# Performance work log

Measured on AMD Instinct MI355X. Metric: run time of the kernel, lower is better.

Reference implementation:

```python
import jax, jax.numpy as jnp
import numpy as np

C = 1.0            # curvature
SEG = 24           # segment_length
S = 14             # lookback // SEG = window_size
PRED_SEGS = 4      # pred_len // SEG
DECAY = 0.9
EPS = 1e-7

# ---- Poincare ball ops ----
def _norm(x):
    return jnp.sqrt(jnp.maximum(jnp.sum(x * x, -1, keepdims=True), EPS * EPS))

def project(x, c=C):
    max_n = (1.0 - 1e-5) / jnp.sqrt(c)
    n = _norm(x)
    return jnp.where(n > max_n, x * (max_n / n), x)

def mobius_add(x, y, c=C):
    x2 = jnp.sum(x * x, -1, keepdims=True)
    y2 = jnp.sum(y * y, -1, keepdims=True)
    xy = jnp.sum(x * y, -1, keepdims=True)
    num = (1 + 2 * c * xy + c * y2) * x + (1 - c * x2) * y
    den = 1 + 2 * c * xy + c * c * x2 * y2
    return num / jnp.maximum(den, 1e-15)

def logmap(x, y, c=C):
    sc = jnp.sqrt(c)
    w = mobius_add(-x, y, c)
    wn = _norm(w)
    lam = 2.0 / jnp.maximum(1.0 - c * jnp.sum(x * x, -1, keepdims=True), EPS)
    return (2.0 / (sc * lam)) * jnp.arctanh(jnp.clip(sc * wn, 0.0, 1.0 - 1e-6)) * w / wn

def expmap(x, v, c=C):
    sc = jnp.sqrt(c)
    vn = _norm(v)
    lam = 2.0 / jnp.maximum(1.0 - c * jnp.sum(x * x, -1, keepdims=True), EPS)
    second = jnp.tanh(sc * lam * vn / 2.0) * v / (sc * vn)
    return project(mobius_add(x, second, c), c)

def expmap0(v, c=C):
    sc = jnp.sqrt(c)
    vn = _norm(v)
    return project(jnp.tanh(sc * vn) * v / (sc * vn), c)

def logmap0(y, c=C):
    sc = jnp.sqrt(c)
    yn = _norm(y)
    return jnp.arctanh(jnp.clip(sc * yn, 0.0, 1.0 - 1e-6)) * y / (sc * yn)


def setup_inputs() -> dict:
    key = jax.random.key(0)
    ks = jax.random.split(key, 16)
    B, L, F = 64, 336, 64
    D, H = 256, 512
    s = 0.02
    inp = {
        "trend": jax.random.normal(ks[0], (B, L, F), jnp.float32),
        "coarse": jax.random.normal(ks[1], (B, L, F), jnp.float32),
        "fine": jax.random.normal(ks[2], (B, L, F), jnp.float32),
        "resid": jax.random.normal(ks[3], (B, L, F), jnp.float32),
        # segment embedding (shared across channels & components)
        "W_emb": jax.random.normal(ks[4], (SEG, D), jnp.float32) * s,
        "b_emb": jnp.zeros((D,), jnp.float32),
        # hyperbolic dynamics MLP: [logmap0(z_last), velocity] -> tangent update
        "W1": jax.random.normal(ks[5], (2 * D, H), jnp.float32) * s,
        "b1": jnp.zeros((H,), jnp.float32),
        "W2": jax.random.normal(ks[6], (H, D), jnp.float32) * s,
        "b2": jnp.zeros((D,), jnp.float32),
        # reconstruction head: tangent -> segment of SEG values
        "Wr1": jax.random.normal(ks[7], (D, H), jnp.float32) * s,
        "br1": jnp.zeros((H,), jnp.float32),
        "Wr2": jax.random.normal(ks[8], (H, SEG), jnp.float32) * s,
        "br2": jnp.zeros((SEG,), jnp.float32),
    }
    return inp


def reference(trend, coarse, fine, resid, W_emb, b_emb, W1, b1, W2, b2, Wr1, br1, Wr2, br2):
    B, L, F = trend.shape
    BF = B * F

    def fold(x):  # [B,L,F] -> [B*F, S, SEG]  (channel-independent)
        return x.transpose(0, 2, 1).reshape(BF, S, SEG)

    def embed(xseg):  # segment -> point on Poincare ball
        return expmap0(jnp.tanh(xseg @ W_emb + b_emb))

    combined = fold(trend + coarse + fine + resid)
    # z_all: [BF, 5, S, D] -- combined, trend, coarse, fine, resid
    z_all = jnp.stack(
        [embed(combined), embed(fold(trend)), embed(fold(coarse)),
         embed(fold(fine)), embed(fold(resid))], axis=1)

    # decayed velocity weights: most recent interval gets decay^0
    w = jnp.power(DECAY, jnp.arange(S - 2, -1, -1).astype(jnp.float32))
    w = w / jnp.sum(w)

    preds = []
    for _ in range(PRED_SEGS):
        # per-interval logmap velocities over the window, all 5 components at once
        vlog = logmap(z_all[:, :, :-1, :], z_all[:, :, 1:, :])   # [BF,5,S-1,D]
        vel = jnp.sum(vlog * w[None, None, :, None], axis=2)      # [BF,5,D]
        z_last = z_all[:, :, -1, :]                               # [BF,5,D]
        # dynamics: tangent-space MLP, step via expmap at z_last
        h = jnp.tanh(jnp.concatenate([logmap0(z_last), vel], -1) @ W1 + b1)
        z_next = expmap(z_last, h @ W2 + b2)                      # [BF,5,D]
        # reconstruct segment from tangent at origin
        r = jax.nn.relu(logmap0(z_next) @ Wr1 + br1) @ Wr2 + br2  # [BF,5,SEG]
        preds.append(r)
        z_all = jnp.concatenate([z_all[:, :, 1:, :], z_next[:, :, None, :]], axis=2)

    out = jnp.stack(preds, axis=2)                  # [BF,5,PRED_SEGS,SEG]
    out = out.reshape(B, F, 5, PRED_SEGS * SEG)     # [B,F,5,pred_len]
    return jnp.transpose(out, (2, 0, 3, 1))         # [5,B,pred_len,F]
```

## Files before the change

kernel.cpp:

```cpp
#include <hip/hip_runtime.h>
#include <cstddef>

#define NSEQ 20480
#define EPSf 1e-7f
#define MAXN 0.99999f
#define MAXN2 (0.99999f * 0.99999f)
#define QCLIP (1.f - MAXN2)
#define GS_CLIP 6.1030949f

typedef __attribute__((ext_vector_type(8))) short bf16x8;
typedef __attribute__((ext_vector_type(4))) float f32x4;

__device__ __forceinline__ unsigned short f2bf(float x) {
  unsigned u = __float_as_uint(x);
  u += 0x7FFF + ((u >> 16) & 1);
  return (unsigned short)(u >> 16);
}
__device__ __forceinline__ float bf2f(unsigned short h) {
  return __uint_as_float(((unsigned)h) << 16);
}
__device__ __forceinline__ void gload16(const void* g, void* l) {
  __builtin_amdgcn_global_load_lds(
      (const __attribute__((address_space(1))) void*)g,
      (__attribute__((address_space(3))) void*)l, 16, 0, 0);
}
__device__ __forceinline__ float fast_exp(float a) {
  return exp2f(a * 1.44269504f);
}
__device__ __forceinline__ float fast_tanh(float a) {
  float e = fast_exp(2.f * a);
  return 1.f - 2.f * __builtin_amdgcn_rcpf(e + 1.f);
}
__device__ __forceinline__ float fast_atanh(float x) {
  return 0.34657359f * log2f((1.f + x) * __builtin_amdgcn_rcpf(1.f - x));
}
__device__ __forceinline__ float sech2f(float a) {
  float u = fast_exp(-2.f * a);
  float om = 1.f + u;
  return 4.f * u * __builtin_amdgcn_rcpf(om * om);
}


__global__ __launch_bounds__(256) void fold_transpose(
    const float* __restrict__ t, const float* __restrict__ c,
    const float* __restrict__ f, const float* __restrict__ r,
    float* __restrict__ XT)
{
  __shared__ float tile[4][56][65];
  const int b = blockIdx.x, l0 = blockIdx.y * 56;
  const int tid = threadIdx.x;
  const int fi = tid & 63, lr0 = tid >> 6;
#pragma unroll
  for (int i = 0; i < 14; ++i) {
    int lr = lr0 + i * 4;
    size_t idx = ((size_t)b * 336 + l0 + lr) * 64 + fi;
    tile[0][lr][fi] = t[idx];
    tile[1][lr][fi] = c[idx];
    tile[2][lr][fi] = f[idx];
    tile[3][lr][fi] = r[idx];
  }
  __syncthreads();
#pragma unroll
  for (int ch = 0; ch < 5; ++ch) {
    for (int i = 0; i < 14; ++i) {
      int idx2 = i * 256 + tid;
      int ff = idx2 / 56, ll = idx2 % 56;
      float v;
      if (ch == 0) v = tile[0][ll][ff] + tile[1][ll][ff] + tile[2][ll][ff] + tile[3][ll][ff];
      else v = tile[ch - 1][ll][ff];
      XT[((size_t)ch * 4096 + (b << 6) + ff) * 336 + l0 + ll] = v;
    }
  }
}

__global__ __launch_bounds__(256) void conv_weight(
    const float* __restrict__ W, unsigned short* __restrict__ Wh, unsigned short* __restrict__ Wl,
    int K, int N, int Nsrc)
{
  int idx = blockIdx.x * 256 + threadIdx.x;
  if (idx >= K * N) return;
  int k = idx / N, n = idx % N;
  float x = (n < Nsrc) ? W[(size_t)k * Nsrc + n] : 0.f;
  unsigned short h = f2bf(x);
  size_t o = ((size_t)(k >> 3) * N + n) * 8 + (k & 7);
  Wh[o] = h;
  if (Wl) Wl[o] = f2bf(x - bf2f(h));
}

__global__ __launch_bounds__(256) void conv_wemb(
    const float* __restrict__ W_emb, unsigned short* __restrict__ WgH, unsigned short* __restrict__ WgL)
{
  int idx = blockIdx.x * 256 + threadIdx.x;
  if (idx >= 16 * 64 * 8) return;
  int j = idx & 7, ln = (idx >> 3) & 63, T = idx >> 9;
  int k = 8 * (ln >> 4) + j, n = T * 16 + (ln & 15);
  float x = (k < 24) ? W_emb[(size_t)k * 256 + n] : 0.f;
  unsigned short h = f2bf(x);
  WgH[idx] = h;
  WgL[idx] = f2bf(x - bf2f(h));
}

__global__ __launch_bounds__(256) void init_kernel(
    const float* __restrict__ XT,
    const unsigned short* __restrict__ WgH, const unsigned short* __restrict__ WgL,
    const float* __restrict__ b_emb,
    unsigned short* __restrict__ Uh, unsigned short* __restrict__ Ul,
    float* __restrict__ ZL, float* __restrict__ QN, unsigned short* __restrict__ VO)
{
  const int tid = threadIdx.x, w = tid >> 6, lane = tid & 63;
  const int l15 = lane & 15, l4 = lane >> 4;
  const int sidx = blockIdx.x * 4 + w;

  bf16x8 ah, al;
  if (l4 < 3) {
    const float* sp = XT + (size_t)sidx * 336 + l15 * 24 + l4 * 8;
    float4 q0 = *(const float4*)sp;
    float4 q1 = *(const float4*)(sp + 4);
    float vv[8] = {q0.x, q0.y, q0.z, q0.w, q1.x, q1.y, q1.z, q1.w};
#pragma unroll
    for (int j = 0; j < 8; ++j) {
      unsigned short h = f2bf(vv[j]);
      ah[j] = (short)h;
      al[j] = (short)f2bf(vv[j] - bf2f(h));
    }
  } else {
#pragma unroll
    for (int j = 0; j < 8; ++j) { ah[j] = 0; al[j] = 0; }
  }

  const bf16x8* BH = (const bf16x8*)WgH;
  const bf16x8* BL = (const bf16x8*)WgL;
  f32x4 acc[16];
#pragma unroll
  for (int T = 0; T < 16; ++T) acc[T] = (f32x4){0.f, 0.f, 0.f, 0.f};
#pragma unroll
  for (int T = 0; T < 16; ++T) {
    bf16x8 bh = BH[T * 64 + lane];
    bf16x8 bl = BL[T * 64 + lane];
    acc[T] = __builtin_amdgcn_mfma_f32_16x16x32_bf16(ah, bh, acc[T], 0, 0, 0);
    acc[T] = __builtin_amdgcn_mfma_f32_16x16x32_bf16(ah, bl, acc[T], 0, 0, 0);
    acc[T] = __builtin_amdgcn_mfma_f32_16x16x32_bf16(al, bh, acc[T], 0, 0, 0);
  }

  float z_[4][16];
  float q_[4];
  float tn_[4];
  float vn_[4];
  float ls[4] = {0.f, 0.f, 0.f, 0.f};
#pragma unroll
  for (int T = 0; T < 16; ++T) {
    float b = b_emb[T * 16 + l15];
#pragma unroll
    for (int r = 0; r < 4; ++r) {
      float e = fast_tanh(acc[T][r] + b);
      z_[r][T] = e;
      ls[r] = fmaf(e, e, ls[r]);
    }
  }
#pragma unroll
  for (int m = 1; m < 16; m <<= 1)
#pragma unroll
    for (int r = 0; r < 4; ++r) ls[r] += __shfl_xor(ls[r], m);
#pragma unroll
  for (int r = 0; r < 4; ++r) {
    float vn = sqrtf(fmaxf(ls[r], 1e-14f));
    float tt = fast_tanh(vn);
    bool clip = tt > MAXN;
    float scale = (clip ? MAXN : tt) / vn;
#pragma unroll
    for (int T = 0; T < 16; ++T) z_[r][T] *= scale;
    tn_[r] = clip ? MAXN : tt;
    vn_[r] = vn;
    q_[r] = clip ? QCLIP : sech2f(vn);
  }

  float zsh[16], qsh;
#pragma unroll
  for (int T = 0; T < 16; ++T) zsh[T] = __shfl(z_[0][T], (lane + 16) & 63);
  qsh = __shfl(q_[0], (lane + 16) & 63);

  float vel[16];
#pragma unroll
  for (int T = 0; T < 16; ++T) vel[T] = 0.f;
  const float p4c = 0.9f * 0.9f * 0.9f * 0.9f;
  const float p8c = p4c * p4c, p12c = p8c * p4c;
  const float wsum = (1.f - p12c * 0.9f) / 0.1f;
  float wt = ((l4 == 0) ? p12c : (l4 == 1) ? p8c : (l4 == 2) ? p4c : 1.f) / wsum;
  const int npairs = (l4 < 3) ? 4 : 1;
#pragma unroll
  for (int p = 0; p < 4; ++p) {
    if (p < npairs) {
      float sd2 = 0.f;
#pragma unroll
      for (int T = 0; T < 16; ++T) {
        float zt1 = (p < 3) ? z_[(p + 1) & 3][T] : zsh[T];
        float d = zt1 - z_[p][T];
        sd2 = fmaf(d, d, sd2);
      }
#pragma unroll
      for (int m = 1; m < 16; m <<= 1) sd2 += __shfl_xor(sd2, m);
      float qx = q_[p];
      float qy = (p < 3) ? q_[(p + 1) & 3] : qsh;
      float den = fmaxf(sd2 + qx * qy, 1e-15f);
      float a2 = (sd2 + qx) / den;
      float b2c = qx / den;
      float wd[16];
      float sww = 0.f;
#pragma unroll
      for (int T = 0; T < 16; ++T) {
        float zt1 = (p < 3) ? z_[(p + 1) & 3][T] : zsh[T];
        wd[T] = b2c * zt1 - a2 * z_[p][T];
        sww = fmaf(wd[T], wd[T], sww);
      }
#pragma unroll
      for (int m = 1; m < 16; m <<= 1) sww += __shfl_xor(sww, m);
      float wn = sqrtf(fmaxf(sww, 1e-14f));
      float vls = qx * fast_atanh(fminf(wn, 1.f - 1e-6f)) / wn;
#pragma unroll
      for (int T = 0; T < 16; ++T) {
        float vl = vls * wd[T];
        vel[T] = fmaf(wt, vl, vel[T]);
        if (l4 == 0 && p < 3)
          VO[((size_t)p * NSEQ + sidx) * 256 + T * 16 + l15] = f2bf(vl);
      }
      wt *= (1.f / 0.9f);
    }
  }

#pragma unroll
  for (int T = 0; T < 16; ++T) {
    vel[T] += __shfl_xor(vel[T], 16);
    vel[T] += __shfl_xor(vel[T], 32);
  }

  if (l4 == 3) {
    float gs = (tn_[1] >= MAXN) ? GS_CLIP : vn_[1] / tn_[1];
#pragma unroll
    for (int T = 0; T < 16; ++T) {
      int cidx = T * 16 + l15;
      float g = gs * z_[1][T];
      size_t o = ((size_t)(cidx >> 3) * NSEQ + sidx) * 8 + (cidx & 7);
      Uh[o] = f2bf(g);
      ZL[(size_t)sidx * 256 + cidx] = z_[1][T];
    }
    if (l15 == 0) QN[sidx] = q_[1];
  }
  if (l4 == 0) {
#pragma unroll
    for (int T = 0; T < 16; ++T) {
      int cidx = 256 + T * 16 + l15;
      unsigned short vh = f2bf(vel[T]);
      size_t o = ((size_t)(cidx >> 3) * NSEQ + sidx) * 8 + (cidx & 7);
      Uh[o] = vh;
      Ul[o] = f2bf(vel[T] - bf2f(vh));
    }
  }
}

template <int EPI>
__global__ __launch_bounds__(256) void gemm_bf16(
    const unsigned short* __restrict__ Ah, int K,
    const unsigned short* __restrict__ Bh, int N,
    const float* __restrict__ bias,
    float* __restrict__ Cf, unsigned short* __restrict__ Ch, int ldc)
{
  __shared__ unsigned short As[8][128][8];
  __shared__ unsigned short Bs[8][128][8];
  const int tid = threadIdx.x;
  const int lane = tid & 63, wid = tid >> 6;
  const int wr = wid >> 1, wc = wid & 1;
  const int l15 = lane & 15, l4 = lane >> 4;
  const int row0 = blockIdx.x * 128, col0 = blockIdx.y * 128;
  unsigned short* As_flat = &As[0][0][0];
  unsigned short* Bs_flat = &Bs[0][0][0];

  f32x4 acc[4][4];
#pragma unroll
  for (int i = 0; i < 4; ++i)
#pragma unroll
    for (int j = 0; j < 4; ++j) acc[i][j] = (f32x4){0.f, 0.f, 0.f, 0.f};

  for (int k0 = 0; k0 < K; k0 += 64) {
    const int kb = k0 >> 3;
#pragma unroll
    for (int rd = 0; rd < 4; ++rd) {
      int c = rd * 256 + tid;
      int kg = c >> 7, m = c & 127;
      gload16(Ah + ((size_t)(kb + kg) * NSEQ + row0 + m) * 8,
              As_flat + (size_t)(rd * 256 + wid * 64) * 8);
    }
#pragma unroll
    for (int rd = 0; rd < 4; ++rd) {
      int c = rd * 256 + tid;
      int kg = c >> 7, n = c & 127;
      gload16(Bh + ((size_t)(kb + kg) * N + col0 + n) * 8,
              Bs_flat + (size_t)(rd * 256 + wid * 64) * 8);
    }
    __syncthreads();

#pragma unroll
    for (int ks = 0; ks < 2; ++ks) {
      bf16x8 fah[4], fbh[4];
#pragma unroll
      for (int mi = 0; mi < 4; ++mi)
        fah[mi] = *(const bf16x8*)&As[ks * 4 + l4][wr * 64 + mi * 16 + l15][0];
#pragma unroll
      for (int ni = 0; ni < 4; ++ni)
        fbh[ni] = *(const bf16x8*)&Bs[ks * 4 + l4][wc * 64 + ni * 16 + l15][0];
#pragma unroll
      for (int mi = 0; mi < 4; ++mi)
#pragma unroll
        for (int ni = 0; ni < 4; ++ni)
          acc[mi][ni] = __builtin_amdgcn_mfma_f32_16x16x32_bf16(fah[mi], fbh[ni], acc[mi][ni], 0, 0, 0);
    }
    __syncthreads();
  }

#pragma unroll
  for (int mi = 0; mi < 4; ++mi)
#pragma unroll
    for (int ni = 0; ni < 4; ++ni) {
      int cc = col0 + wc * 64 + ni * 16 + l15;
      float bv = bias[cc];
      int rbase = row0 + wr * 64 + mi * 16 + l4 * 4;
#pragma unroll
      for (int r = 0; r < 4; ++r) {
        float v = acc[mi][ni][r] + bv;
        if (EPI == 1) v = tanhf(v);
        else if (EPI == 2) v = fmaxf(v, 0.f);
        if (EPI == 0) {
          Cf[(size_t)(rbase + r) * ldc + cc] = v;
        } else {
          size_t o = ((size_t)(cc >> 3) * NSEQ + rbase + r) * 8 + (cc & 7);
          Ch[o] = f2bf(v);
        }
      }
    }
}

__device__ __forceinline__ float wave_sum_f(float v) {
#pragma unroll
  for (int off = 32; off > 0; off >>= 1) v += __shfl_xor(v, off);
  return v;
}

__global__ __launch_bounds__(256) void step_kernel(
    const unsigned short* __restrict__ Vh, unsigned short* __restrict__ Uh, unsigned short* __restrict__ Ul,
    float* __restrict__ ZL, float* __restrict__ QN, const unsigned short* __restrict__ VOk, int k)
{
  const int tid = threadIdx.x, w = tid >> 6, lane = tid & 63;
  const int sidx = blockIdx.x * 4 + w;

  float x[4], v[4];
#pragma unroll
  for (int j = 0; j < 4; ++j) {
    int d = lane + 64 * j;
    x[j] = ZL[(size_t)sidx * 256 + d];
    v[j] = bf2f(Vh[((size_t)(d >> 3) * NSEQ + sidx) * 8 + (d & 7)]);
  }
  float qx = QN[sidx];

  float svv = 0.f;
#pragma unroll
  for (int j = 0; j < 4; ++j) svv = fmaf(v[j], v[j], svv);
  float vn2 = wave_sum_f(svv);
  float vn = sqrtf(fmaxf(vn2, 1e-14f));
  float arg = vn / qx;
  float th = fast_tanh(arg);
  float sec_s = th / vn;
  float qsec = sech2f(arg);

  float ssp = 0.f;
#pragma unroll
  for (int j = 0; j < 4; ++j) {
    float s = fmaf(sec_s, v[j], x[j]);
    ssp = fmaf(s, s, ssp);
  }
  float s2p = wave_sum_f(ssp);
  float den = fmaxf(s2p + qx * qsec, 1e-15f);
  float alpha = (s2p + qx) / den;
  float beta = qx * sec_s / den;

  float zn[4];
  float snn = 0.f;
#pragma unroll
  for (int j = 0; j < 4; ++j) {
    zn[j] = alpha * x[j] + beta * v[j];
    snn = fmaf(zn[j], zn[j], snn);
  }
  float n2 = wave_sum_f(snn);
  float n = sqrtf(fmaxf(n2, 1e-14f));
  bool clip = n > MAXN;
  float scl = clip ? MAXN / n : 1.f;
  float qz = clip ? QCLIP : (1.f - n2);
#pragma unroll
  for (int j = 0; j < 4; ++j) {
    zn[j] *= scl;
    ZL[(size_t)sidx * 256 + lane + 64 * j] = zn[j];
  }
  if (lane == 0) QN[sidx] = qz;

  float gs;
  if (clip) gs = GS_CLIP;
  else {
    float opn = 1.f + n;
    gs = 0.34657359f * log2f(opn * opn * __builtin_amdgcn_rcpf(qz)) / n;
  }
#pragma unroll
  for (int j = 0; j < 4; ++j) {
    int d = lane + 64 * j;
    float g = gs * zn[j];
    size_t o = ((size_t)(d >> 3) * NSEQ + sidx) * 8 + (d & 7);
    Uh[o] = f2bf(g);
  }

  if (k < 3) {
    float sdd = 0.f;
#pragma unroll
    for (int j = 0; j < 4; ++j) {
      float d = zn[j] - x[j];
      sdd = fmaf(d, d, sdd);
    }
    float sd2b = wave_sum_f(sdd);
    float den2 = fmaxf(sd2b + qx * qz, 1e-15f);
    float a2 = (sd2b + qx) / den2;
    float b2 = qx / den2;
    float wv[4];
    float sww = 0.f;
#pragma unroll
    for (int j = 0; j < 4; ++j) {
      wv[j] = b2 * zn[j] - a2 * x[j];
      sww = fmaf(wv[j], wv[j], sww);
    }
    float wn2 = wave_sum_f(sww);
    float wn = sqrtf(fmaxf(wn2, 1e-14f));
    float vls = qx * fast_atanh(fminf(wn, 1.f - 1e-6f)) / wn;

    float p12 = 1.f;
#pragma unroll
    for (int i = 0; i < 12; ++i) p12 *= 0.9f;
    float wsum = (1.f - p12 * 0.9f) / 0.1f;
    float w0 = p12 / wsum;
    float w12 = 1.f / wsum;
#pragma unroll
    for (int j = 0; j < 4; ++j) {
      int dd = 256 + lane + 64 * j;
      size_t o = ((size_t)(dd >> 3) * NSEQ + sidx) * 8 + (dd & 7);
      float velold = bf2f(Uh[o]) + bf2f(Ul[o]);
      float vdrop = bf2f(VOk[(size_t)sidx * 256 + lane + 64 * j]);
      float velnew = 0.9f * (velold - w0 * vdrop) + w12 * (vls * wv[j]);
      unsigned short vh = f2bf(velnew);
      Uh[o] = vh;
      Ul[o] = f2bf(velnew - bf2f(vh));
    }
  }
}

__global__ __launch_bounds__(256) void gemm4_mfma(
    const unsigned short* __restrict__ Ah,
    const unsigned short* __restrict__ Bh,
    const float* __restrict__ br2, float* __restrict__ out, int step)
{
  __shared__ unsigned short As[4][128][8];
  __shared__ unsigned short Bs[4][32][8];
  const int tid = threadIdx.x, lane = tid & 63, wid = tid >> 6;
  const int l15 = lane & 15, l4 = lane >> 4;
  const int row0 = blockIdx.x * 128;
  unsigned short* As_flat = &As[0][0][0];
  unsigned short* Bs_flat = &Bs[0][0][0];

  f32x4 acc[2][2];
#pragma unroll
  for (int i = 0; i < 2; ++i)
#pragma unroll
    for (int j = 0; j < 2; ++j) acc[i][j] = (f32x4){0.f, 0.f, 0.f, 0.f};

  for (int k0 = 0; k0 < 512; k0 += 32) {
    const int kb = k0 >> 3;
#pragma unroll
    for (int rd = 0; rd < 2; ++rd) {
      int c = rd * 256 + tid;
      int kg = c >> 7, m = c & 127;
      gload16(Ah + ((size_t)(kb + kg) * NSEQ + row0 + m) * 8,
              As_flat + (size_t)(rd * 256 + wid * 64) * 8);
    }
    if (tid < 128) {
      int kg = tid >> 5, n = tid & 31;
      gload16(Bh + ((size_t)(kb + kg) * 32 + n) * 8,
              Bs_flat + (size_t)(wid * 64) * 8);
    }
    __syncthreads();

    bf16x8 fah[2], fbh[2];
#pragma unroll
    for (int mi = 0; mi < 2; ++mi)
      fah[mi] = *(const bf16x8*)&As[l4][wid * 32 + mi * 16 + l15][0];
#pragma unroll
    for (int ni = 0; ni < 2; ++ni)
      fbh[ni] = *(const bf16x8*)&Bs[l4][ni * 16 + l15][0];
#pragma unroll
    for (int mi = 0; mi < 2; ++mi)
#pragma unroll
      for (int ni = 0; ni < 2; ++ni)
        acc[mi][ni] = __builtin_amdgcn_mfma_f32_16x16x32_bf16(fah[mi], fbh[ni], acc[mi][ni], 0, 0, 0);
    __syncthreads();
  }

#pragma unroll
  for (int mi = 0; mi < 2; ++mi)
#pragma unroll
    for (int ni = 0; ni < 2; ++ni) {
      int j = ni * 16 + l15;
      if (j < 24) {
        float bv = br2[j];
#pragma unroll
        for (int r = 0; r < 4; ++r) {
          int row = row0 + wid * 32 + mi * 16 + l4 * 4 + r;
          int c = row >> 12, bf = row & 4095, b = bf >> 6, f = bf & 63;
          size_t base = (((size_t)(c * 64 + b) * 96) + (size_t)step * 24 + j) * 64 + f;
          out[base] = acc[mi][ni][r] + bv;
        }
      }
    }
}

extern "C" void kernel_launch(void* const* d_in, const int* in_sizes, int n_in,
                              void* d_out, int out_size, void* d_ws, size_t ws_size,
                              hipStream_t stream)
{
  const float* trend  = (const float*)d_in[0];
  const float* coarse = (const float*)d_in[1];
  const float* fine   = (const float*)d_in[2];
  const float* resid  = (const float*)d_in[3];
  const float* W_emb  = (const float*)d_in[4];
  const float* b_emb  = (const float*)d_in[5];
  const float* W1  = (const float*)d_in[6];
  const float* b1  = (const float*)d_in[7];
  const float* W2  = (const float*)d_in[8];
  const float* b2  = (const float*)d_in[9];
  const float* Wr1 = (const float*)d_in[10];
  const float* br1 = (const float*)d_in[11];
  const float* Wr2 = (const float*)d_in[12];
  const float* br2 = (const float*)d_in[13];
  float* out = (float*)d_out;

  char* p = (char*)d_ws;
  size_t off = 0;
  auto alloc = [&](size_t bytes) -> void* {
    void* r = p + off;
    off = (off + bytes + 255) & ~(size_t)255;
    return r;
  };
  unsigned short* Uh = (unsigned short*)alloc((size_t)NSEQ * 512 * 2);
  unsigned short* Ul = (unsigned short*)alloc((size_t)NSEQ * 512 * 2);
  unsigned short* Hh = (unsigned short*)alloc((size_t)NSEQ * 512 * 2);
  unsigned short* Vh = (unsigned short*)alloc((size_t)NSEQ * 256 * 2);
  float* ZL  = (float*)alloc((size_t)NSEQ * 256 * 4);
  float* QN  = (float*)alloc((size_t)NSEQ * 4);
  unsigned short* VO = (unsigned short*)alloc((size_t)3 * NSEQ * 256 * 2);
  float* XT  = (float*)alloc((size_t)5 * 4096 * 336 * 4);
  unsigned short* W1h = (unsigned short*)alloc((size_t)512 * 512 * 2);
  unsigned short* W2h = (unsigned short*)alloc((size_t)512 * 256 * 2);
  unsigned short* Wr1h = (unsigned short*)alloc((size_t)256 * 512 * 2);
  unsigned short* Wr2h = (unsigned short*)alloc((size_t)512 * 32 * 2);
  unsigned short* WgH = (unsigned short*)alloc((size_t)16 * 64 * 8 * 2);
  unsigned short* WgL = (unsigned short*)alloc((size_t)16 * 64 * 8 * 2);

  fold_transpose<<<dim3(64, 6), 256, 0, stream>>>(trend, coarse, fine, resid, XT);
  conv_weight<<<(512 * 512 + 255) / 256, 256, 0, stream>>>(W1, W1h, nullptr, 512, 512, 512);
  conv_weight<<<(512 * 256 + 255) / 256, 256, 0, stream>>>(W2, W2h, nullptr, 512, 256, 256);
  conv_weight<<<(256 * 512 + 255) / 256, 256, 0, stream>>>(Wr1, Wr1h, nullptr, 256, 512, 512);
  conv_weight<<<(512 * 32 + 255) / 256, 256, 0, stream>>>(Wr2, Wr2h, nullptr, 512, 32, 24);
  conv_wemb<<<32, 256, 0, stream>>>(W_emb, WgH, WgL);
  init_kernel<<<NSEQ / 4, 256, 0, stream>>>(XT, WgH, WgL, b_emb, Uh, Ul, ZL, QN, VO);

  for (int k = 0; k < 4; ++k) {
    gemm_bf16<1><<<dim3(160, 4), 256, 0, stream>>>(Uh, 512, W1h, 512, b1, nullptr, Hh, 512);
    gemm_bf16<3><<<dim3(160, 2), 256, 0, stream>>>(Hh, 512, W2h, 256, b2, nullptr, Vh, 256);
    const unsigned short* vok = VO + (size_t)(k < 3 ? k : 0) * NSEQ * 256;
    step_kernel<<<NSEQ / 4, 256, 0, stream>>>(Vh, Uh, Ul, ZL, QN, vok, k);
    gemm_bf16<2><<<dim3(160, 4), 256, 0, stream>>>(Uh, 256, Wr1h, 512, br1, nullptr, Hh, 512);
    gemm4_mfma<<<160, 256, 0, stream>>>(Hh, Wr2h, br2, out, k);
  }
}
```

Before: 518.5 us.

## Fuse W2 GEMM with hyperbolic step kernel into one full-row MFMA kernel

Replaces the separate W2 GEMM and the per-sequence step kernel with a single kernel. Each block computes 64 full rows of the 256-wide output, so the row-wise norms, expmap, projection and velocity update can run straight from the accumulators. This removes the bf16 Vh intermediate and one kernel launch per step. In exchange, only 320 blocks are launched, the kernel carries larger register state (16 accumulators plus 64 x values per lane), and the ZL/Uh stores are less coalesced, which may lower occupancy.

```diff
diff --git a/kernel.cpp b/kernel.cpp
--- a/kernel.cpp
+++ b/kernel.cpp
@@ -262,7 +262,7 @@
     const unsigned short* __restrict__ Ah, int K,
     const unsigned short* __restrict__ Bh, int N,
     const float* __restrict__ bias,
-    float* __restrict__ Cf, unsigned short* __restrict__ Ch, int ldc)
+    unsigned short* __restrict__ Ch)
 {
   __shared__ unsigned short As[8][128][8];
   __shared__ unsigned short Bs[8][128][8];
@@ -327,114 +327,205 @@
       for (int r = 0; r < 4; ++r) {
         float v = acc[mi][ni][r] + bv;
         if (EPI == 1) v = tanhf(v);
-        else if (EPI == 2) v = fmaxf(v, 0.f);
-        if (EPI == 0) {
-          Cf[(size_t)(rbase + r) * ldc + cc] = v;
-        } else {
-          size_t o = ((size_t)(cc >> 3) * NSEQ + rbase + r) * 8 + (cc & 7);
-          Ch[o] = f2bf(v);
-        }
-      }
-    }
-}
-
-__device__ __forceinline__ float wave_sum_f(float v) {
-#pragma unroll
-  for (int off = 32; off > 0; off >>= 1) v += __shfl_xor(v, off);
-  return v;
-}
-
-__global__ __launch_bounds__(256) void step_kernel(
-    const unsigned short* __restrict__ Vh, unsigned short* __restrict__ Uh, unsigned short* __restrict__ Ul,
-    float* __restrict__ ZL, float* __restrict__ QN, const unsigned short* __restrict__ VOk, int k)
-{
-  const int tid = threadIdx.x, w = tid >> 6, lane = tid & 63;
-  const int sidx = blockIdx.x * 4 + w;
-
-  float x[4], v[4];
-#pragma unroll
-  for (int j = 0; j < 4; ++j) {
-    int d = lane + 64 * j;
-    x[j] = ZL[(size_t)sidx * 256 + d];
-    v[j] = bf2f(Vh[((size_t)(d >> 3) * NSEQ + sidx) * 8 + (d & 7)]);
-  }
-  float qx = QN[sidx];
-
-  float svv = 0.f;
-#pragma unroll
-  for (int j = 0; j < 4; ++j) svv = fmaf(v[j], v[j], svv);
-  float vn2 = wave_sum_f(svv);
-  float vn = sqrtf(fmaxf(vn2, 1e-14f));
-  float arg = vn / qx;
-  float th = fast_tanh(arg);
-  float sec_s = th / vn;
-  float qsec = sech2f(arg);
-
-  float ssp = 0.f;
-#pragma unroll
-  for (int j = 0; j < 4; ++j) {
-    float s = fmaf(sec_s, v[j], x[j]);
-    ssp = fmaf(s, s, ssp);
-  }
-  float s2p = wave_sum_f(ssp);
-  float den = fmaxf(s2p + qx * qsec, 1e-15f);
-  float alpha = (s2p + qx) / den;
-  float beta = qx * sec_s / den;
-
-  float zn[4];
-  float snn = 0.f;
-#pragma unroll
-  for (int j = 0; j < 4; ++j) {
-    zn[j] = alpha * x[j] + beta * v[j];
-    snn = fmaf(zn[j], zn[j], snn);
-  }
-  float n2 = wave_sum_f(snn);
-  float n = sqrtf(fmaxf(n2, 1e-14f));
-  bool clip = n > MAXN;
-  float scl = clip ? MAXN / n : 1.f;
-  float qz = clip ? QCLIP : (1.f - n2);
-#pragma unroll
-  for (int j = 0; j < 4; ++j) {
-    zn[j] *= scl;
-    ZL[(size_t)sidx * 256 + lane + 64 * j] = zn[j];
-  }
-  if (lane == 0) QN[sidx] = qz;
-
-  float gs;
-  if (clip) gs = GS_CLIP;
-  else {
-    float opn = 1.f + n;
-    gs = 0.34657359f * log2f(opn * opn * __builtin_amdgcn_rcpf(qz)) / n;
-  }
-#pragma unroll
-  for (int j = 0; j < 4; ++j) {
-    int d = lane + 64 * j;
-    float g = gs * zn[j];
-    size_t o = ((size_t)(d >> 3) * NSEQ + sidx) * 8 + (d & 7);
-    Uh[o] = f2bf(g);
+        else v = fmaxf(v, 0.f);
+        size_t o = ((size_t)(cc >> 3) * NSEQ + rbase + r) * 8 + (cc & 7);
+        Ch[o] = f2bf(v);
+      }
+    }
+}
+
+__global__ __launch_bounds__(256) void gemm2_step(
+    const unsigned short* __restrict__ Hh,
+    const unsigned short* __restrict__ W2h,
+    const float* __restrict__ b2,
+    unsigned short* __restrict__ Uh, unsigned short* __restrict__ Ul,
+    float* __restrict__ ZL, float* __restrict__ QN,
+    const unsigned short* __restrict__ VOk, int k)
+{
+  __shared__ unsigned short As[8][64][8];
+  __shared__ unsigned short Bs[8][256][8];
+  const int tid = threadIdx.x, lane = tid & 63, wid = tid >> 6;
+  const int l15 = lane & 15, l4 = lane >> 4;
+  const int row0 = blockIdx.x * 64;
+  unsigned short* As_flat = &As[0][0][0];
+  unsigned short* Bs_flat = &Bs[0][0][0];
+
+  f32x4 acc[16];
+#pragma unroll
+  for (int ni = 0; ni < 16; ++ni) acc[ni] = (f32x4){0.f, 0.f, 0.f, 0.f};
+
+  for (int k0 = 0; k0 < 512; k0 += 64) {
+    const int kb = k0 >> 3;
+#pragma unroll
+    for (int rd = 0; rd < 2; ++rd) {
+      int c = rd * 256 + tid;
+      int kg = c >> 6, m = c & 63;
+      gload16(Hh + ((size_t)(kb + kg) * NSEQ + row0 + m) * 8,
+              As_flat + (size_t)(rd * 256 + wid * 64) * 8);
+    }
+#pragma unroll
+    for (int rd = 0; rd < 8; ++rd) {
+      int c = rd * 256 + tid;
+      int kg = c >> 8, n = c & 255;
+      gload16(W2h + ((size_t)(kb + kg) * 256 + n) * 8,
+              Bs_flat + (size_t)(rd * 256 + wid * 64) * 8);
+    }
+    __syncthreads();
+
+#pragma unroll
+    for (int ks = 0; ks < 2; ++ks) {
+      bf16x8 fa = *(const bf16x8*)&As[ks * 4 + l4][wid * 16 + l15][0];
+#pragma unroll
+      for (int ni = 0; ni < 16; ++ni) {
+        bf16x8 fb = *(const bf16x8*)&Bs[ks * 4 + l4][ni * 16 + l15][0];
+        acc[ni] = __builtin_amdgcn_mfma_f32_16x16x32_bf16(fa, fb, acc[ni], 0, 0, 0);
+      }
+    }
+    __syncthreads();
+  }
+
+  const int rowb = row0 + wid * 16 + l4 * 4;
+  float x_[4][16];
+  float qx[4];
+#pragma unroll
+  for (int r = 0; r < 4; ++r) {
+    qx[r] = QN[rowb + r];
+#pragma unroll
+    for (int ni = 0; ni < 16; ++ni)
+      x_[r][ni] = ZL[(size_t)(rowb + r) * 256 + ni * 16 + l15];
+  }
+
+  float svv[4] = {0.f, 0.f, 0.f, 0.f};
+#pragma unroll
+  for (int ni = 0; ni < 16; ++ni) {
+    float bv = b2[ni * 16 + l15];
+#pragma unroll
+    for (int r = 0; r < 4; ++r) {
+      float vv = acc[ni][r] + bv;
+      acc[ni][r] = vv;
+      svv[r] = fmaf(vv, vv, svv[r]);
+    }
+  }
+#pragma unroll
+  for (int m = 1; m < 16; m <<= 1)
+#pragma unroll
+    for (int r = 0; r < 4; ++r) svv[r] += __shfl_xor(svv[r], m);
+
+  float sec_s[4], qsec[4];
+#pragma unroll
+  for (int r = 0; r < 4; ++r) {
+    float vn = sqrtf(fmaxf(svv[r], 1e-14f));
+    float arg = vn / qx[r];
+    float th = fast_tanh(arg);
+    sec_s[r] = th / vn;
+    qsec[r] = sech2f(arg);
+  }
+
+  float ssp[4] = {0.f, 0.f, 0.f, 0.f};
+#pragma unroll
+  for (int ni = 0; ni < 16; ++ni)
+#pragma unroll
+    for (int r = 0; r < 4; ++r) {
+      float s = fmaf(sec_s[r], acc[ni][r], x_[r][ni]);
+      ssp[r] = fmaf(s, s, ssp[r]);
+    }
+#pragma unroll
+  for (int m = 1; m < 16; m <<= 1)
+#pragma unroll
+    for (int r = 0; r < 4; ++r) ssp[r] += __shfl_xor(ssp[r], m);
+
+  float alpha[4], beta[4];
+#pragma unroll
+  for (int r = 0; r < 4; ++r) {
+    float den = fmaxf(ssp[r] + qx[r] * qsec[r], 1e-15f);
+    alpha[r] = (ssp[r] + qx[r]) / den;
+    beta[r] = qx[r] * sec_s[r] / den;
+  }
+
+  float snn[4] = {0.f, 0.f, 0.f, 0.f};
+#pragma unroll
+  for (int ni = 0; ni < 16; ++ni)
+#pragma unroll
+    for (int r = 0; r < 4; ++r) {
+      float zn = fmaf(alpha[r], x_[r][ni], beta[r] * acc[ni][r]);
+      acc[ni][r] = zn;
+      snn[r] = fmaf(zn, zn, snn[r]);
+    }
+#pragma unroll
+  for (int m = 1; m < 16; m <<= 1)
+#pragma unroll
+    for (int r = 0; r < 4; ++r) snn[r] += __shfl_xor(snn[r], m);
+
+  float scl[4], qz[4], gs[4];
+#pragma unroll
+  for (int r = 0; r < 4; ++r) {
+    float n = sqrtf(fmaxf(snn[r], 1e-14f));
+    bool clip = n > MAXN;
+    scl[r] = clip ? MAXN / n : 1.f;
+    qz[r] = clip ? QCLIP : (1.f - snn[r]);
+    if (clip) gs[r] = GS_CLIP;
+    else {
+      float opn = 1.f + n;
+      gs[r] = 0.34657359f * log2f(opn * opn * __builtin_amdgcn_rcpf(qz[r])) / n;
+    }
+  }
+
+#pragma unroll
+  for (int ni = 0; ni < 16; ++ni)
+#pragma unroll
+    for (int r = 0; r < 4; ++r) {
+      float zn = acc[ni][r] * scl[r];
+      acc[ni][r] = zn;
+      ZL[(size_t)(rowb + r) * 256 + ni * 16 + l15] = zn;
+      int d = ni * 16 + l15;
+      Uh[((size_t)(d >> 3) * NSEQ + rowb + r) * 8 + (d & 7)] = f2bf(gs[r] * zn);
+    }
+  if (l15 == 0) {
+#pragma unroll
+    for (int r = 0; r < 4; ++r) QN[rowb + r] = qz[r];
   }
 
   if (k < 3) {
-    float sdd = 0.f;
-#pragma unroll
-    for (int j = 0; j < 4; ++j) {
-      float d = zn[j] - x[j];
-      sdd = fmaf(d, d, sdd);
-    }
-    float sd2b = wave_sum_f(sdd);
-    float den2 = fmaxf(sd2b + qx * qz, 1e-15f);
-    float a2 = (sd2b + qx) / den2;
-    float b2 = qx / den2;
-    float wv[4];
-    float sww = 0.f;
-#pragma unroll
-    for (int j = 0; j < 4; ++j) {
-      wv[j] = b2 * zn[j] - a2 * x[j];
-      sww = fmaf(wv[j], wv[j], sww);
-    }
-    float wn2 = wave_sum_f(sww);
-    float wn = sqrtf(fmaxf(wn2, 1e-14f));
-    float vls = qx * fast_atanh(fminf(wn, 1.f - 1e-6f)) / wn;
+    float sdd[4] = {0.f, 0.f, 0.f, 0.f};
+#pragma unroll
+    for (int ni = 0; ni < 16; ++ni)
+#pragma unroll
+      for (int r = 0; r < 4; ++r) {
+        float d = acc[ni][r] - x_[r][ni];
+        sdd[r] = fmaf(d, d, sdd[r]);
+      }
+#pragma unroll
+    for (int m = 1; m < 16; m <<= 1)
+#pragma unroll
+      for (int r = 0; r < 4; ++r) sdd[r] += __shfl_xor(sdd[r], m);
+
+    float a2[4], b2c[4];
+#pragma unroll
+    for (int r = 0; r < 4; ++r) {
+      float den2 = fmaxf(sdd[r] + qx[r] * qz[r], 1e-15f);
+      a2[r] = (sdd[r] + qx[r]) / den2;
+      b2c[r] = qx[r] / den2;
+    }
+    float sww[4] = {0.f, 0.f, 0.f, 0.f};
+#pragma unroll
+    for (int ni = 0; ni < 16; ++ni)
+#pragma unroll
+      for (int r = 0; r < 4; ++r) {
+        float wv = b2c[r] * acc[ni][r] - a2[r] * x_[r][ni];
+        x_[r][ni] = wv;
+        sww[r] = fmaf(wv, wv, sww[r]);
+      }
+#pragma unroll
+    for (int m = 1; m < 16; m <<= 1)
+#pragma unroll
+      for (int r = 0; r < 4; ++r) sww[r] += __shfl_xor(sww[r], m);
+
+    float vls[4];
+#pragma unroll
+    for (int r = 0; r < 4; ++r) {
+      float wn = sqrtf(fmaxf(sww[r], 1e-14f));
+      vls[r] = qx[r] * fast_atanh(fminf(wn, 1.f - 1e-6f)) / wn;
+    }
 
     float p12 = 1.f;
 #pragma unroll
@@ -443,16 +534,18 @@
     float w0 = p12 / wsum;
     float w12 = 1.f / wsum;
 #pragma unroll
-    for (int j = 0; j < 4; ++j) {
-      int dd = 256 + lane + 64 * j;
-      size_t o = ((size_t)(dd >> 3) * NSEQ + sidx) * 8 + (dd & 7);
-      float velold = bf2f(Uh[o]) + bf2f(Ul[o]);
-      float vdrop = bf2f(VOk[(size_t)sidx * 256 + lane + 64 * j]);
-      float velnew = 0.9f * (velold - w0 * vdrop) + w12 * (vls * wv[j]);
-      unsigned short vh = f2bf(velnew);
-      Uh[o] = vh;
-      Ul[o] = f2bf(velnew - bf2f(vh));
-    }
+    for (int ni = 0; ni < 16; ++ni)
+#pragma unroll
+      for (int r = 0; r < 4; ++r) {
+        int dd = 256 + ni * 16 + l15;
+        size_t o = ((size_t)(dd >> 3) * NSEQ + rowb + r) * 8 + (dd & 7);
+        float velold = bf2f(Uh[o]) + bf2f(Ul[o]);
+        float vdrop = bf2f(VOk[(size_t)(rowb + r) * 256 + ni * 16 + l15]);
+        float velnew = 0.9f * (velold - w0 * vdrop) + w12 * (vls[r] * x_[r][ni]);
+        unsigned short vh = f2bf(velnew);
+        Uh[o] = vh;
+        Ul[o] = f2bf(velnew - bf2f(vh));
+      }
   }
 }
 
@@ -554,7 +647,6 @@
   unsigned short* Uh = (unsigned short*)alloc((size_t)NSEQ * 512 * 2);
   unsigned short* Ul = (unsigned short*)alloc((size_t)NSEQ * 512 * 2);
   unsigned short* Hh = (unsigned short*)alloc((size_t)NSEQ * 512 * 2);
-  unsigned short* Vh = (unsigned short*)alloc((size_t)NSEQ * 256 * 2);
   float* ZL  = (float*)alloc((size_t)NSEQ * 256 * 4);
   float* QN  = (float*)alloc((size_t)NSEQ * 4);
   unsigned short* VO = (unsigned short*)alloc((size_t)3 * NSEQ * 256 * 2);
@@ -575,11 +667,10 @@
   init_kernel<<<NSEQ / 4, 256, 0, stream>>>(XT, WgH, WgL, b_emb, Uh, Ul, ZL, QN, VO);
 
   for (int k = 0; k < 4; ++k) {
-    gemm_bf16<1><<<dim3(160, 4), 256, 0, stream>>>(Uh, 512, W1h, 512, b1, nullptr, Hh, 512);
-    gemm_bf16<3><<<dim3(160, 2), 256, 0, stream>>>(Hh, 512, W2h, 256, b2, nullptr, Vh, 256);
+    gemm_bf16<1><<<dim3(160, 4), 256, 0, stream>>>(Uh, 512, W1h, 512, b1, Hh);
     const unsigned short* vok = VO + (size_t)(k < 3 ? k : 0) * NSEQ * 256;
-    step_kernel<<<NSEQ / 4, 256, 0, stream>>>(Vh, Uh, Ul, ZL, QN, vok, k);
-    gemm_bf16<2><<<dim3(160, 4), 256, 0, stream>>>(Uh, 256, Wr1h, 512, br1, nullptr, Hh, 512);
+    gemm2_step<<<NSEQ / 64, 256, 0, stream>>>(Hh, W2h, b2, Uh, Ul, ZL, QN, vok, k);
+    gemm_bf16<2><<<dim3(160, 4), 256, 0, stream>>>(Uh, 256, Wr1h, 512, br1, Hh);
     gemm4_mfma<<<160, 256, 0, stream>>>(Hh, Wr2h, br2, out, k);
   }
 }
```

Result: slower. 600.9 us (+15.9%).
